# Kernel tuning notes

Measured on AMD Instinct MI355X. Metric: run time of the kernel, lower is better.

The kernel has to match this reference:

```python
import jax, jax.numpy as jnp
import numpy as np

SIGMA = 1.5
KSIZE = 3
CROP = 5

def _gaussian_window():
    # matches cv2.getGaussianKernel(3, 1.5): normalized 1D gaussian, outer product
    g = np.exp(-((np.arange(KSIZE) - (KSIZE - 1) / 2.0) ** 2) / (2.0 * SIGMA ** 2))
    g = g / g.sum()
    return np.outer(g, g)  # (3, 3)

def _filt(img, win):
    # img: [B, W, H, C]; 3x3 depthwise correlation with BORDER_REFLECT_101 (= jnp 'reflect')
    C = img.shape[-1]
    p = jnp.pad(img, ((0, 0), (1, 1), (1, 1), (0, 0)), mode='reflect')
    k = jnp.broadcast_to(win[:, :, None, None], (KSIZE, KSIZE, 1, C)).astype(img.dtype)
    return jax.lax.conv_general_dilated(
        p, k, window_strides=(1, 1), padding='VALID',
        dimension_numbers=('NHWC', 'HWIO', 'NHWC'), feature_group_count=C)

def setup_inputs() -> dict:
    key = jax.random.key(0)
    k1, k2 = jax.random.split(key)
    X = jax.random.uniform(k1, (32, 3, 512, 512), dtype=jnp.float32) * 255.0
    Y = jax.random.uniform(k2, (32, 3, 512, 512), dtype=jnp.float32) * 255.0
    return {"X": X, "Y": Y}

def reference(X, Y):
    B, C, W, H = X.shape
    # source does numpy reshape (c,w,h)->(w,h,c); replicate exactly
    x = X.reshape(B, W, H, C)
    y = Y.reshape(B, W, H, C)
    win = jnp.asarray(_gaussian_window(), dtype=X.dtype)
    c = slice(CROP, -CROP)
    mu1 = _filt(x, win)[:, c, c, :]
    mu2 = _filt(y, win)[:, c, c, :]
    sigma1_sq = _filt(x * x, win)[:, c, c, :] - mu1 * mu1
    sigma2_sq = _filt(y * y, win)[:, c, c, :] - mu2 * mu2
    sigma12 = _filt(x * y, win)[:, c, c, :] - mu1 * mu2
    loss = sigma1_sq + sigma2_sq - 2.0 * sigma12  # local variance of (x - y)
    return jnp.sum(jnp.mean(loss, axis=(1, 2, 3)))
```

## Files before the change

### kernel.cpp

```cpp
#include <hip/hip_runtime.h>


constexpr int Wd     = 512;
constexpr int Hd     = 512;
constexpr int Cd     = 3;
constexpr int ROW    = Hd * Cd;
constexpr int CROPc  = 5;
constexpr int NOUTc  = Wd - 2 * CROPc;
constexpr int HC_LO  = 15;
constexpr int HC_HI  = 1520;
constexpr int OUT_PER_WAVE = 58;
constexpr int NHCW   = (NOUTc * Cd + OUT_PER_WAVE - 1) / OUT_PER_WAVE;
constexpr int NCHUNK = 8;
constexpr int CHUNKc = 63;
constexpr int BLOCK  = 256;
constexpr int NWAVES = 32 * NCHUNK * NHCW;
constexpr int NBLK   = NWAVES / (BLOCK / 64);
static_assert(NWAVES % (BLOCK / 64) == 0, "");

__global__ __launch_bounds__(BLOCK) void locvar_kernel(
    const float* __restrict__ X,
    const float* __restrict__ Y,
    float* __restrict__ partial)
{
    const int lane = threadIdx.x & 63;
    const int widx = threadIdx.x >> 6;
    const int gw   = blockIdx.x * (BLOCK / 64) + widx;

    const int hcw   = gw % NHCW;
    const int rest  = gw / NHCW;
    const int chunk = rest % NCHUNK;
    const int b     = rest / NCHUNK;

    const int hc = 12 + OUT_PER_WAVE * hcw + lane;
    const int w0 = CROPc + chunk * CHUNKc;
    const int wn = min(CHUNKc, CROPc + NOUTc - w0);

    const bool valid = (lane >= 3) && (lane <= 60) && (hc >= HC_LO) && (hc <= HC_HI);
    const float vmask = valid ? 1.0f : 0.0f;

    const float e  = expf(-1.0f / 4.5f);
    const float g1 = 1.0f / (1.0f + 2.0f * e);
    const float g0 = e * g1;

    const int am = ((lane - 3) & 63) << 2;
    const int ap = ((lane + 3) & 63) << 2;

    const size_t base = (size_t)b * Wd * ROW + (size_t)hc;

#define ROWSUMS(OFF, Rr, Qq)                                                     \
    {                                                                            \
        float dd  = X[(OFF)] - Y[(OFF)];                                         \
        float dmv = __int_as_float(                                              \
            __builtin_amdgcn_ds_bpermute(am, __float_as_int(dd)));               \
        float dpv = __int_as_float(                                              \
            __builtin_amdgcn_ds_bpermute(ap, __float_as_int(dd)));               \
        Rr = g0 * (dmv + dpv) + g1 * dd;                                         \
        Qq = g0 * fmaf(dpv, dpv, dmv * dmv) + g1 * (dd * dd);                    \
    }

    float R0, R1, Q0, Q1;
    {
        size_t off = base + (size_t)(w0 - 1) * ROW;
        ROWSUMS(off, R0, Q0);
        off += ROW;
        ROWSUMS(off, R1, Q1);
    }

    float acc = 0.0f;
    size_t off = base + (size_t)(w0 + 1) * ROW;
    #pragma unroll 2
    for (int i = 0; i < wn; ++i, off += ROW) {
        float R2, Q2;
        ROWSUMS(off, R2, Q2);

        float S1 = g0 * (R0 + R2) + g1 * R1;
        float S2 = g0 * (Q0 + Q2) + g1 * Q1;
        acc += vmask * fmaf(-S1, S1, S2);

        R0 = R1; R1 = R2;
        Q0 = Q1; Q1 = Q2;
    }
#undef ROWSUMS

    #pragma unroll
    for (int o = 32; o > 0; o >>= 1) acc += __shfl_down(acc, o, 64);

    __shared__ float sdata[BLOCK / 64];
    if (lane == 0) sdata[widx] = acc;
    __syncthreads();
    if (threadIdx.x == 0) {
        float s = 0.0f;
        #pragma unroll
        for (int i = 0; i < BLOCK / 64; ++i) s += sdata[i];
        partial[blockIdx.x] = s;
    }
}

__global__ __launch_bounds__(BLOCK) void reduce_kernel(
    const float* __restrict__ partial,
    float* __restrict__ out)
{
    float acc = 0.0f;
    for (int i = threadIdx.x; i < NBLK; i += BLOCK) acc += partial[i];

    #pragma unroll
    for (int o = 32; o > 0; o >>= 1) acc += __shfl_down(acc, o, 64);

    __shared__ float sdata[BLOCK / 64];
    const int lane = threadIdx.x & 63;
    const int wid  = threadIdx.x >> 6;
    if (lane == 0) sdata[wid] = acc;
    __syncthreads();
    if (threadIdx.x == 0) {
        float s = 0.0f;
        #pragma unroll
        for (int i = 0; i < BLOCK / 64; ++i) s += sdata[i];
        out[0] = s * (1.0f / ((float)NOUTc * (float)NOUTc * (float)Cd));
    }
}

extern "C" void kernel_launch(void* const* d_in, const int* in_sizes, int n_in,
                              void* d_out, int out_size, void* d_ws, size_t ws_size,
                              hipStream_t stream) {
    const float* X = (const float*)d_in[0];
    const float* Y = (const float*)d_in[1];
    float* out     = (float*)d_out;
    float* partial = (float*)d_ws;

    locvar_kernel<<<NBLK, BLOCK, 0, stream>>>(X, Y, partial);
    reduce_kernel<<<1, BLOCK, 0, stream>>>(partial, out);
}
```

Measured before the change: 42.48 us.

## Vectorize loads to float4 per lane with wider column windows and shorter row chunks

Each lane now loads four consecutive floats with float4 loads instead of one scalar, so a wave covers a 256-wide column window (246 valid outputs) rather than 58. Horizontal neighbours are fetched with six bpermutes per row instead of two per element, and per-element masks handle window edges. The work split becomes 7 column windows by 24 row chunks of 21 rows. This cuts the number of load instructions and the fraction of halo lanes that load data but produce no output, at the cost of more registers and a longer row-halo overhead per chunk.

After: 45.17 us. 1.06x slower.

```diff
diff --git a/kernel.cpp b/kernel.cpp
--- a/kernel.cpp
+++ b/kernel.cpp
@@ -9,12 +9,13 @@
 constexpr int NOUTc  = Wd - 2 * CROPc;
 constexpr int HC_LO  = 15;
 constexpr int HC_HI  = 1520;
-constexpr int OUT_PER_WAVE = 58;
-constexpr int NHCW   = (NOUTc * Cd + OUT_PER_WAVE - 1) / OUT_PER_WAVE;
-constexpr int NCHUNK = 8;
-constexpr int CHUNKc = 63;
+
+constexpr int NWIN   = 7;
+constexpr int OUTW   = 246;
+constexpr int NCHUNK = 24;
+constexpr int CHUNKc = 21;
 constexpr int BLOCK  = 256;
-constexpr int NWAVES = 32 * NCHUNK * NHCW;
+constexpr int NWAVES = 32 * NCHUNK * NWIN;
 constexpr int NBLK   = NWAVES / (BLOCK / 64);
 static_assert(NWAVES % (BLOCK / 64) == 0, "");
 
@@ -27,39 +28,59 @@
     const int widx = threadIdx.x >> 6;
     const int gw   = blockIdx.x * (BLOCK / 64) + widx;
 
-    const int hcw   = gw % NHCW;
-    const int rest  = gw / NHCW;
+    const int win   = gw % NWIN;
+    const int rest  = gw / NWIN;
     const int chunk = rest % NCHUNK;
     const int b     = rest / NCHUNK;
 
-    const int hc = 12 + OUT_PER_WAVE * hcw + lane;
+    const int o_lo = HC_LO + OUTW * win;
+    const int o_hi = min(o_lo + OUTW - 1, HC_HI);
+    const int s    = (o_lo - 3) & ~3;
+    const int idx0 = s + 4 * lane;
+
     const int w0 = CROPc + chunk * CHUNKc;
     const int wn = min(CHUNKc, CROPc + NOUTc - w0);
 
-    const bool valid = (lane >= 3) && (lane <= 60) && (hc >= HC_LO) && (hc <= HC_HI);
-    const float vmask = valid ? 1.0f : 0.0f;
+    float4 msk;
+    msk.x = (idx0 + 0 >= o_lo && idx0 + 0 <= o_hi) ? 1.0f : 0.0f;
+    msk.y = (idx0 + 1 >= o_lo && idx0 + 1 <= o_hi) ? 1.0f : 0.0f;
+    msk.z = (idx0 + 2 >= o_lo && idx0 + 2 <= o_hi) ? 1.0f : 0.0f;
+    msk.w = (idx0 + 3 >= o_lo && idx0 + 3 <= o_hi) ? 1.0f : 0.0f;
 
     const float e  = expf(-1.0f / 4.5f);
     const float g1 = 1.0f / (1.0f + 2.0f * e);
     const float g0 = e * g1;
 
-    const int am = ((lane - 3) & 63) << 2;
-    const int ap = ((lane + 3) & 63) << 2;
+    const int am = ((lane - 1) & 63) << 2;
+    const int ap = ((lane + 1) & 63) << 2;
 
-    const size_t base = (size_t)b * Wd * ROW + (size_t)hc;
+    const size_t base = (size_t)b * Wd * ROW + (size_t)idx0;
 
-#define ROWSUMS(OFF, Rr, Qq)                                                     \
-    {                                                                            \
-        float dd  = X[(OFF)] - Y[(OFF)];                                         \
-        float dmv = __int_as_float(                                              \
-            __builtin_amdgcn_ds_bpermute(am, __float_as_int(dd)));               \
-        float dpv = __int_as_float(                                              \
-            __builtin_amdgcn_ds_bpermute(ap, __float_as_int(dd)));               \
-        Rr = g0 * (dmv + dpv) + g1 * dd;                                         \
-        Qq = g0 * fmaf(dpv, dpv, dmv * dmv) + g1 * (dd * dd);                    \
+#define BPERM(A, V) __int_as_float(__builtin_amdgcn_ds_bpermute((A), __float_as_int(V)))
+
+#define ROWSUMS(OFF, Rr, Qq)                                                   \
+    {                                                                          \
+        float4 x4 = *reinterpret_cast<const float4*>(X + (OFF));               \
+        float4 y4 = *reinterpret_cast<const float4*>(Y + (OFF));               \
+        float4 d;                                                              \
+        d.x = x4.x - y4.x; d.y = x4.y - y4.y;                                  \
+        d.z = x4.z - y4.z; d.w = x4.w - y4.w;                                  \
+        float pm1 = BPERM(am, d.y), pm2 = BPERM(am, d.z), pm3 = BPERM(am, d.w);\
+        float np0 = BPERM(ap, d.x), np1 = BPERM(ap, d.y), np2 = BPERM(ap, d.z);\
+        float4 dm, dp;                                                         \
+        dm.x = pm1; dm.y = pm2; dm.z = pm3; dm.w = d.x;                        \
+        dp.x = d.w; dp.y = np0; dp.z = np1; dp.w = np2;                        \
+        Rr.x = fmaf(g0, dm.x + dp.x, g1 * d.x);                                \
+        Rr.y = fmaf(g0, dm.y + dp.y, g1 * d.y);                                \
+        Rr.z = fmaf(g0, dm.z + dp.z, g1 * d.z);                                \
+        Rr.w = fmaf(g0, dm.w + dp.w, g1 * d.w);                                \
+        Qq.x = fmaf(g0, fmaf(dp.x, dp.x, dm.x * dm.x), g1 * (d.x * d.x));      \
+        Qq.y = fmaf(g0, fmaf(dp.y, dp.y, dm.y * dm.y), g1 * (d.y * d.y));      \
+        Qq.z = fmaf(g0, fmaf(dp.z, dp.z, dm.z * dm.z), g1 * (d.z * d.z));      \
+        Qq.w = fmaf(g0, fmaf(dp.w, dp.w, dm.w * dm.w), g1 * (d.w * d.w));      \
     }
 
-    float R0, R1, Q0, Q1;
+    float4 R0, R1, Q0, Q1;
     {
         size_t off = base + (size_t)(w0 - 1) * ROW;
         ROWSUMS(off, R0, Q0);
@@ -67,33 +88,47 @@
         ROWSUMS(off, R1, Q1);
     }
 
-    float acc = 0.0f;
+    float4 acc = {0.0f, 0.0f, 0.0f, 0.0f};
     size_t off = base + (size_t)(w0 + 1) * ROW;
-    #pragma unroll 2
+    #pragma unroll 3
     for (int i = 0; i < wn; ++i, off += ROW) {
-        float R2, Q2;
+        float4 R2, Q2;
         ROWSUMS(off, R2, Q2);
 
-        float S1 = g0 * (R0 + R2) + g1 * R1;
-        float S2 = g0 * (Q0 + Q2) + g1 * Q1;
-        acc += vmask * fmaf(-S1, S1, S2);
+        float4 S1, S2;
+        S1.x = fmaf(g0, R0.x + R2.x, g1 * R1.x);
+        S1.y = fmaf(g0, R0.y + R2.y, g1 * R1.y);
+        S1.z = fmaf(g0, R0.z + R2.z, g1 * R1.z);
+        S1.w = fmaf(g0, R0.w + R2.w, g1 * R1.w);
+        S2.x = fmaf(g0, Q0.x + Q2.x, g1 * Q1.x);
+        S2.y = fmaf(g0, Q0.y + Q2.y, g1 * Q1.y);
+        S2.z = fmaf(g0, Q0.z + Q2.z, g1 * Q1.z);
+        S2.w = fmaf(g0, Q0.w + Q2.w, g1 * Q1.w);
+
+        acc.x = fmaf(msk.x, fmaf(-S1.x, S1.x, S2.x), acc.x);
+        acc.y = fmaf(msk.y, fmaf(-S1.y, S1.y, S2.y), acc.y);
+        acc.z = fmaf(msk.z, fmaf(-S1.z, S1.z, S2.z), acc.z);
+        acc.w = fmaf(msk.w, fmaf(-S1.w, S1.w, S2.w), acc.w);
 
         R0 = R1; R1 = R2;
         Q0 = Q1; Q1 = Q2;
     }
 #undef ROWSUMS
+#undef BPERM
+
+    float a = (acc.x + acc.y) + (acc.z + acc.w);
 
     #pragma unroll
-    for (int o = 32; o > 0; o >>= 1) acc += __shfl_down(acc, o, 64);
+    for (int o = 32; o > 0; o >>= 1) a += __shfl_down(a, o, 64);
 
     __shared__ float sdata[BLOCK / 64];
-    if (lane == 0) sdata[widx] = acc;
+    if (lane == 0) sdata[widx] = a;
     __syncthreads();
     if (threadIdx.x == 0) {
-        float s = 0.0f;
+        float sum = 0.0f;
         #pragma unroll
-        for (int i = 0; i < BLOCK / 64; ++i) s += sdata[i];
-        partial[blockIdx.x] = s;
+        for (int i = 0; i < BLOCK / 64; ++i) sum += sdata[i];
+        partial[blockIdx.x] = sum;
     }
 }
 
```

## Vectorize loads to float4 with multi-segment waves and explicit row prefetch

Applied to the files above, without the earlier changes.

Restructures the sliding-window kernel so each lane handles four adjacent elements via float4 loads, and each wave covers three or four horizontal segments across row bands of 16. Loads for the next row are issued before the current row's compute (double-buffered register pipeline), and lane shuffles shift by one lane instead of three. The goal is wider memory transactions, more in-flight loads per thread, and less halo overhead per wave. In exchange it raises register pressure and increases the halo re-reads from the shorter row bands, and the grid shrinks to 512 blocks.

New measurement: 40.99 us. -3.5%, faster.

```diff
diff --git a/kernel.cpp b/kernel.cpp
--- a/kernel.cpp
+++ b/kernel.cpp
@@ -1,99 +1,166 @@
 #include <hip/hip_runtime.h>
 
 
-constexpr int Wd     = 512;
-constexpr int Hd     = 512;
-constexpr int Cd     = 3;
-constexpr int ROW    = Hd * Cd;
-constexpr int CROPc  = 5;
-constexpr int NOUTc  = Wd - 2 * CROPc;
-constexpr int HC_LO  = 15;
-constexpr int HC_HI  = 1520;
-constexpr int OUT_PER_WAVE = 58;
-constexpr int NHCW   = (NOUTc * Cd + OUT_PER_WAVE - 1) / OUT_PER_WAVE;
-constexpr int NCHUNK = 8;
-constexpr int CHUNKc = 63;
-constexpr int BLOCK  = 256;
-constexpr int NWAVES = 32 * NCHUNK * NHCW;
-constexpr int NBLK   = NWAVES / (BLOCK / 64);
-static_assert(NWAVES % (BLOCK / 64) == 0, "");
-
-__global__ __launch_bounds__(BLOCK) void locvar_kernel(
+constexpr int ROW   = 1536;
+constexpr int IMG   = 512 * ROW;
+constexpr int BLOCK = 256;
+constexpr int CH    = 16;
+constexpr int NBLK  = 32 * 2 * 8;
+
+__device__ __forceinline__ float bperm(int addr, float v) {
+    return __int_as_float(__builtin_amdgcn_ds_bpermute(addr, __float_as_int(v)));
+}
+
+__global__ __launch_bounds__(BLOCK, 2) void locvar_kernel(
     const float* __restrict__ X,
     const float* __restrict__ Y,
     float* __restrict__ partial)
 {
     const int lane = threadIdx.x & 63;
     const int widx = threadIdx.x >> 6;
-    const int gw   = blockIdx.x * (BLOCK / 64) + widx;
-
-    const int hcw   = gw % NHCW;
-    const int rest  = gw / NHCW;
-    const int chunk = rest % NCHUNK;
-    const int b     = rest / NCHUNK;
-
-    const int hc = 12 + OUT_PER_WAVE * hcw + lane;
-    const int w0 = CROPc + chunk * CHUNKc;
-    const int wn = min(CHUNKc, CROPc + NOUTc - w0);
-
-    const bool valid = (lane >= 3) && (lane <= 60) && (hc >= HC_LO) && (hc <= HC_HI);
-    const float vmask = valid ? 1.0f : 0.0f;
+    const int blk  = blockIdx.x;
+    const int q    = blk & 7;
+    const int half = (blk >> 3) & 1;
+    const int b    = blk >> 4;
+
+    const int band = q * 4 + widx;
+    const int w0   = 5 + CH * band;
+    const int wn   = min(CH, 507 - w0);
+
+    const int nw   = 3 + half;
+    const int HLO  = half ? 753 : 15;
+    const int OUTW = half ? 192 : 246;
 
     const float e  = expf(-1.0f / 4.5f);
     const float g1 = 1.0f / (1.0f + 2.0f * e);
     const float g0 = e * g1;
 
-    const int am = ((lane - 3) & 63) << 2;
-    const int ap = ((lane + 3) & 63) << 2;
-
-    const size_t base = (size_t)b * Wd * ROW + (size_t)hc;
-
-#define ROWSUMS(OFF, Rr, Qq)                                                     \
-    {                                                                            \
-        float dd  = X[(OFF)] - Y[(OFF)];                                         \
-        float dmv = __int_as_float(                                              \
-            __builtin_amdgcn_ds_bpermute(am, __float_as_int(dd)));               \
-        float dpv = __int_as_float(                                              \
-            __builtin_amdgcn_ds_bpermute(ap, __float_as_int(dd)));               \
-        Rr = g0 * (dmv + dpv) + g1 * dd;                                         \
-        Qq = g0 * fmaf(dpv, dpv, dmv * dmv) + g1 * (dd * dd);                    \
-    }
-
-    float R0, R1, Q0, Q1;
-    {
-        size_t off = base + (size_t)(w0 - 1) * ROW;
-        ROWSUMS(off, R0, Q0);
-        off += ROW;
-        ROWSUMS(off, R1, Q1);
-    }
-
-    float acc = 0.0f;
-    size_t off = base + (size_t)(w0 + 1) * ROW;
-    #pragma unroll 2
-    for (int i = 0; i < wn; ++i, off += ROW) {
-        float R2, Q2;
-        ROWSUMS(off, R2, Q2);
-
-        float S1 = g0 * (R0 + R2) + g1 * R1;
-        float S2 = g0 * (Q0 + Q2) + g1 * Q1;
-        acc += vmask * fmaf(-S1, S1, S2);
-
-        R0 = R1; R1 = R2;
-        Q0 = Q1; Q1 = Q2;
-    }
+    const int am = ((lane - 1) & 63) << 2;
+    const int ap = ((lane + 1) & 63) << 2;
+
+    int gbase[4];
+    float4 msk[4];
+    #pragma unroll
+    for (int j = 0; j < 4; ++j) {
+        const int o_lo = HLO + OUTW * j;
+        const int o_hi = o_lo + OUTW - 1;
+        const int s    = (o_lo - 3) & ~3;
+        const int idx0 = s + 4 * lane;
+        gbase[j] = b * IMG + idx0;
+        msk[j].x = (idx0 + 0 >= o_lo && idx0 + 0 <= o_hi) ? 1.0f : 0.0f;
+        msk[j].y = (idx0 + 1 >= o_lo && idx0 + 1 <= o_hi) ? 1.0f : 0.0f;
+        msk[j].z = (idx0 + 2 >= o_lo && idx0 + 2 <= o_hi) ? 1.0f : 0.0f;
+        msk[j].w = (idx0 + 3 >= o_lo && idx0 + 3 <= o_hi) ? 1.0f : 0.0f;
+    }
+
+    float4 xa[4], ya[4], xb[4], yb[4];
+    float4 R0[4], R1[4], Q0[4], Q1[4];
+    float4 acc = {0.0f, 0.0f, 0.0f, 0.0f};
+
+#define LOADROW(DX, DY, R)                                                      \
+    {                                                                           \
+        const int ro = (R) * ROW;                                               \
+        _Pragma("unroll")                                                       \
+        for (int j = 0; j < 4; ++j) if (j < nw) {                               \
+            DX[j] = *reinterpret_cast<const float4*>(X + gbase[j] + ro);        \
+            DY[j] = *reinterpret_cast<const float4*>(Y + gbase[j] + ro);        \
+        }                                                                       \
+    }
+
+#define ROWSUMS(SX, SY, RA, QA)                                                 \
+    {                                                                           \
+        _Pragma("unroll")                                                       \
+        for (int j = 0; j < 4; ++j) if (j < nw) {                               \
+            float4 d;                                                           \
+            d.x = SX[j].x - SY[j].x; d.y = SX[j].y - SY[j].y;                   \
+            d.z = SX[j].z - SY[j].z; d.w = SX[j].w - SY[j].w;                   \
+            float pm1 = bperm(am, d.y), pm2 = bperm(am, d.z),                   \
+                  pm3 = bperm(am, d.w);                                         \
+            float np0 = bperm(ap, d.x), np1 = bperm(ap, d.y),                   \
+                  np2 = bperm(ap, d.z);                                         \
+            float4 dm, dp;                                                      \
+            dm.x = pm1; dm.y = pm2; dm.z = pm3; dm.w = d.x;                     \
+            dp.x = d.w; dp.y = np0; dp.z = np1; dp.w = np2;                     \
+            RA[j].x = fmaf(g0, dm.x + dp.x, g1 * d.x);                          \
+            RA[j].y = fmaf(g0, dm.y + dp.y, g1 * d.y);                          \
+            RA[j].z = fmaf(g0, dm.z + dp.z, g1 * d.z);                          \
+            RA[j].w = fmaf(g0, dm.w + dp.w, g1 * d.w);                          \
+            QA[j].x = fmaf(g0, fmaf(dp.x, dp.x, dm.x * dm.x), g1 * (d.x * d.x));\
+            QA[j].y = fmaf(g0, fmaf(dp.y, dp.y, dm.y * dm.y), g1 * (d.y * d.y));\
+            QA[j].z = fmaf(g0, fmaf(dp.z, dp.z, dm.z * dm.z), g1 * (d.z * d.z));\
+            QA[j].w = fmaf(g0, fmaf(dp.w, dp.w, dm.w * dm.w), g1 * (d.w * d.w));\
+        }                                                                       \
+    }
+
+#define PHASE(SX, SY, RNEXT)                                                    \
+    {                                                                           \
+        _Pragma("unroll")                                                       \
+        for (int j = 0; j < 4; ++j) if (j < nw) {                               \
+            float4 d, R2, Q2;                                                   \
+            d.x = SX[j].x - SY[j].x; d.y = SX[j].y - SY[j].y;                   \
+            d.z = SX[j].z - SY[j].z; d.w = SX[j].w - SY[j].w;                   \
+            float pm1 = bperm(am, d.y), pm2 = bperm(am, d.z),                   \
+                  pm3 = bperm(am, d.w);                                         \
+            float np0 = bperm(ap, d.x), np1 = bperm(ap, d.y),                   \
+                  np2 = bperm(ap, d.z);                                         \
+            float4 dm, dp;                                                      \
+            dm.x = pm1; dm.y = pm2; dm.z = pm3; dm.w = d.x;                     \
+            dp.x = d.w; dp.y = np0; dp.z = np1; dp.w = np2;                     \
+            R2.x = fmaf(g0, dm.x + dp.x, g1 * d.x);                             \
+            R2.y = fmaf(g0, dm.y + dp.y, g1 * d.y);                             \
+            R2.z = fmaf(g0, dm.z + dp.z, g1 * d.z);                             \
+            R2.w = fmaf(g0, dm.w + dp.w, g1 * d.w);                             \
+            Q2.x = fmaf(g0, fmaf(dp.x, dp.x, dm.x * dm.x), g1 * (d.x * d.x));   \
+            Q2.y = fmaf(g0, fmaf(dp.y, dp.y, dm.y * dm.y), g1 * (d.y * d.y));   \
+            Q2.z = fmaf(g0, fmaf(dp.z, dp.z, dm.z * dm.z), g1 * (d.z * d.z));   \
+            Q2.w = fmaf(g0, fmaf(dp.w, dp.w, dm.w * dm.w), g1 * (d.w * d.w));   \
+            float4 S1, S2;                                                      \
+            S1.x = fmaf(g0, R0[j].x + R2.x, g1 * R1[j].x);                      \
+            S1.y = fmaf(g0, R0[j].y + R2.y, g1 * R1[j].y);                      \
+            S1.z = fmaf(g0, R0[j].z + R2.z, g1 * R1[j].z);                      \
+            S1.w = fmaf(g0, R0[j].w + R2.w, g1 * R1[j].w);                      \
+            S2.x = fmaf(g0, Q0[j].x + Q2.x, g1 * Q1[j].x);                      \
+            S2.y = fmaf(g0, Q0[j].y + Q2.y, g1 * Q1[j].y);                      \
+            S2.z = fmaf(g0, Q0[j].z + Q2.z, g1 * Q1[j].z);                      \
+            S2.w = fmaf(g0, Q0[j].w + Q2.w, g1 * Q1[j].w);                      \
+            acc.x = fmaf(msk[j].x, fmaf(-S1.x, S1.x, S2.x), acc.x);             \
+            acc.y = fmaf(msk[j].y, fmaf(-S1.y, S1.y, S2.y), acc.y);             \
+            acc.z = fmaf(msk[j].z, fmaf(-S1.z, S1.z, S2.z), acc.z);             \
+            acc.w = fmaf(msk[j].w, fmaf(-S1.w, S1.w, S2.w), acc.w);             \
+            R0[j] = R1[j]; R1[j] = R2;                                          \
+            Q0[j] = Q1[j]; Q1[j] = Q2;                                          \
+        }                                                                       \
+        LOADROW(SX, SY, RNEXT);                                                 \
+    }
+
+    LOADROW(xa, ya, w0 - 1);
+    LOADROW(xb, yb, w0);
+    ROWSUMS(xa, ya, R0, Q0);
+    LOADROW(xa, ya, w0 + 1);
+    ROWSUMS(xb, yb, R1, Q1);
+    LOADROW(xb, yb, w0 + 2);
+
+    for (int i = 0; i < wn; i += 2) {
+        PHASE(xa, ya, min(w0 + 3 + i, w0 + wn));
+        PHASE(xb, yb, min(w0 + 4 + i, w0 + wn));
+    }
+#undef PHASE
 #undef ROWSUMS
+#undef LOADROW
+
+    float a = (acc.x + acc.y) + (acc.z + acc.w);
 
     #pragma unroll
-    for (int o = 32; o > 0; o >>= 1) acc += __shfl_down(acc, o, 64);
+    for (int o = 32; o > 0; o >>= 1) a += __shfl_down(a, o, 64);
 
     __shared__ float sdata[BLOCK / 64];
-    if (lane == 0) sdata[widx] = acc;
+    if (lane == 0) sdata[widx] = a;
     __syncthreads();
     if (threadIdx.x == 0) {
-        float s = 0.0f;
+        float sum = 0.0f;
         #pragma unroll
-        for (int i = 0; i < BLOCK / 64; ++i) s += sdata[i];
-        partial[blockIdx.x] = s;
+        for (int i = 0; i < BLOCK / 64; ++i) sum += sdata[i];
+        partial[blockIdx.x] = sum;
     }
 }
 
@@ -116,7 +183,7 @@
         float s = 0.0f;
         #pragma unroll
         for (int i = 0; i < BLOCK / 64; ++i) s += sdata[i];
-        out[0] = s * (1.0f / ((float)NOUTc * (float)NOUTc * (float)Cd));
+        out[0] = s * (1.0f / (502.0f * 502.0f * 3.0f));
     }
 }
 
```
